# Performance work log

Measured on AMD Instinct MI355X. Metric: run time of the kernel, lower is better.

Reference implementation:

```python
import jax, jax.numpy as jnp
import numpy as np

B = 8192; N = 50; NUM_NODES = 200000; NUM_EDGES = 1000000
FEAT = 64; EFEAT = 4; TD = 16; D = 64


def setup_inputs() -> dict:
    key = jax.random.key(0)
    ks = jax.random.split(key, 32)
    p = lambda i, shape: jax.random.normal(ks[i], shape, jnp.float32) * 0.05
    inp = {}
    nf = jax.random.normal(ks[0], (NUM_NODES, FEAT), jnp.float32)
    skills = jax.random.randint(ks[1], (NUM_NODES,), 0, 100).astype(jnp.float32)
    inp['node_raw_features'] = nf.at[:, 0].set(skills)  # col 0 = skill id
    inp['edge_raw_features'] = jax.random.normal(ks[2], (NUM_EDGES, EFEAT), jnp.float32)
    inp['src_node_ids'] = jax.random.randint(ks[3], (B,), 0, NUM_NODES)
    inp['dst_node_ids'] = jax.random.randint(ks[4], (B,), 0, NUM_NODES)
    inp['node_interact_times'] = jax.random.uniform(ks[5], (B,), jnp.float32, 0.0, 1e4)
    inp['src_neighbor_node_ids'] = jax.random.randint(ks[6], (B, N), 0, NUM_NODES)
    inp['src_neighbor_edge_ids'] = jax.random.randint(ks[7], (B, N), 0, NUM_EDGES)
    inp['src_neighbor_times'] = jax.random.uniform(ks[8], (B, N), jnp.float32, 0.0, 1e4)
    inp['dst_neighbor_node_ids'] = jax.random.randint(ks[9], (B, N), 0, NUM_NODES)
    inp['dst_neighbor_edge_ids'] = jax.random.randint(ks[10], (B, N), 0, NUM_EDGES)
    inp['dst_neighbor_times'] = jax.random.uniform(ks[11], (B, N), jnp.float32, 0.0, 1e4)
    # projection layers
    inp['W_feat'] = p(12, (FEAT, D)); inp['b_feat'] = p(13, (D,))
    inp['W_edge'] = p(14, (1, D));    inp['b_edge'] = p(15, (D,))
    inp['W_time'] = p(16, (TD, D));   inp['b_time'] = p(17, (D,))
    inp['W_struct'] = p(18, (1, D));  inp['b_struct'] = p(19, (D,))
    inp['W_out'] = p(20, (D, D));     inp['b_out'] = p(21, (D,))
    # time encoder (cos(w*dt + b), trainable Linear(1, TD) as in TGN TimeEncoder)
    inp['time_w'] = p(22, (TD,)); inp['time_b'] = p(23, (TD,))
    # src / dst GRUs (PyTorch layout: W_ih [3H,E], W_hh [3H,H])
    inp['src_W_ih'] = p(24, (3 * D, D)); inp['src_W_hh'] = p(25, (3 * D, D))
    inp['src_b_ih'] = p(26, (3 * D,));   inp['src_b_hh'] = p(27, (3 * D,))
    inp['dst_W_ih'] = p(28, (3 * D, D)); inp['dst_W_hh'] = p(29, (3 * D, D))
    inp['dst_b_ih'] = p(30, (3 * D,));   inp['dst_b_hh'] = p(31, (3 * D,))
    return inp


def _lin(x, W, b):
    return x @ W + b


def _gru_last_hidden(x, W_ih, W_hh, b_ih, b_hh):
    # x: [B, T, E] -> final hidden state [B, H] (PyTorch GRU equations)
    Bb, _, _ = x.shape
    H = W_hh.shape[1]

    def step(h, xt):
        gi = xt @ W_ih.T + b_ih            # [B, 3H]
        gh = h @ W_hh.T + b_hh             # [B, 3H]
        ir, iz, inn = jnp.split(gi, 3, axis=-1)
        hr, hz, hn = jnp.split(gh, 3, axis=-1)
        r = jax.nn.sigmoid(ir + hr)
        z = jax.nn.sigmoid(iz + hz)
        n = jnp.tanh(inn + r * hn)
        h_new = (1.0 - z) * n + z * h
        return h_new, None

    h0 = jnp.zeros((Bb, H), x.dtype)
    hT, _ = jax.lax.scan(step, h0, jnp.swapaxes(x, 0, 1))
    return hT


def reference(node_raw_features, edge_raw_features, src_node_ids, dst_node_ids,
              node_interact_times, src_neighbor_node_ids, src_neighbor_edge_ids,
              src_neighbor_times, dst_neighbor_node_ids, dst_neighbor_edge_ids,
              dst_neighbor_times, W_feat, b_feat, W_edge, b_edge, W_time, b_time,
              W_struct, b_struct, W_out, b_out, time_w, time_b,
              src_W_ih, src_W_hh, src_b_ih, src_b_hh,
              dst_W_ih, dst_W_hh, dst_b_ih, dst_b_hh):
    t = node_interact_times
    # append the query interaction itself (edge id 0) -> [B, N+1]
    src_nids = jnp.concatenate([src_neighbor_node_ids, src_node_ids[:, None]], 1)
    src_eids = jnp.concatenate([src_neighbor_edge_ids, jnp.zeros_like(src_node_ids)[:, None]], 1)
    src_ts = jnp.concatenate([src_neighbor_times, t[:, None]], 1)
    dst_nids = jnp.concatenate([dst_neighbor_node_ids, dst_node_ids[:, None]], 1)
    dst_eids = jnp.concatenate([dst_neighbor_edge_ids, jnp.zeros_like(dst_node_ids)[:, None]], 1)
    dst_ts = jnp.concatenate([dst_neighbor_times, t[:, None]], 1)

    # co-occurrence features [B, N, 1]
    co_src = (src_neighbor_node_ids == dst_node_ids[:, None]).astype(jnp.float32)[..., None]
    co_dst = (dst_neighbor_node_ids == src_node_ids[:, None]).astype(jnp.float32)[..., None]
    # skill match features [B, N, 1]
    src_skill = node_raw_features[src_nids][:, :-1, 0].astype(jnp.int32)
    dst_skill = node_raw_features[dst_nids][:, -1, 0].astype(jnp.int32)[:, None]
    skill_f = (src_skill == dst_skill).astype(jnp.float32)[..., None]

    src_struct = _lin(co_src, W_struct, b_struct)
    dst_struct = _lin(co_dst, W_struct, b_struct)
    skill_struct = _lin(skill_f, W_struct, b_struct)

    def get_feats(nids, eids, ts):
        node_f = _lin(node_raw_features[nids], W_feat, b_feat)        # [B,N+1,D]
        delta = t[:, None] - ts                                       # dual-decay ablation: delta times
        tenc = jnp.cos(delta[..., None] * time_w + time_b)            # [B,N+1,TD]
        time_f = _lin(tenc, W_time, b_time)                           # [B,N+1,D]
        edge_f = _lin(edge_raw_features[eids][..., :1], W_edge, b_edge)
        return node_f, edge_f, time_f

    sn, se, st = get_feats(src_nids, src_eids, src_ts)
    dn, de, dt = get_feats(dst_nids, dst_eids, dst_ts)
    src_feats = sn + se + st
    dst_feats = dn + de + dt

    src_emb = _gru_last_hidden(src_feats[:, :-1] + skill_struct + src_struct,
                               src_W_ih, src_W_hh, src_b_ih, src_b_hh) + (se + st)[:, -1]
    dst_emb = _gru_last_hidden((de + dt)[:, :-1] + dst_struct,
                               dst_W_ih, dst_W_hh, dst_b_ih, dst_b_hh) + dst_feats[:, -1]

    return _lin(src_emb, W_out, b_out), _lin(dst_emb, W_out, b_out)
```

## Files before the change

kernel.cpp:

```cpp
#include <hip/hip_runtime.h>
#include <stdint.h>

#define BB 8192
#define NN 50

typedef _Float16 half8 __attribute__((ext_vector_type(8)));
typedef float floatx4 __attribute__((ext_vector_type(4)));

union FragU { uint4 u; half8 h; };
static __device__ __forceinline__ half8 u2h(uint4 u) { FragU f; f.u = u; return f.h; }

static __device__ __forceinline__ uint32_t pk2u(float a, float b) {
    auto p = __builtin_amdgcn_cvt_pkrtz(a, b);
    uint32_t u; __builtin_memcpy(&u, &p, 4); return u;
}

#define MFMA(A, B, C) __builtin_amdgcn_mfma_f32_16x16x32_f16((A), (B), (C), 0, 0, 0)

static __device__ __forceinline__ float frcp(float x) {
#if __has_builtin(__builtin_amdgcn_rcpf)
    return __builtin_amdgcn_rcpf(x);
#else
    return 1.0f / x;
#endif
}
static __device__ __forceinline__ float fexp2(float x) {
#if __has_builtin(__builtin_amdgcn_exp2f)
    return __builtin_amdgcn_exp2f(x);
#else
    return __expf(0.69314718056f * x);
#endif
}
static __device__ __forceinline__ float fsig(float x)   { return frcp(1.0f + fexp2(-1.44269504089f * x)); }
static __device__ __forceinline__ float ftanhf(float x) { return 1.0f - 2.0f * frcp(fexp2(2.88539008178f * x) + 1.0f); }

static __device__ __forceinline__ void bar_lds() {
    asm volatile("s_waitcnt lgkmcnt(0)" ::: "memory");
    __builtin_amdgcn_s_barrier();
}

__global__ __launch_bounds__(128, 2)
void dygkt4(const float* __restrict__ nodef, const float* __restrict__ edgef,
            const int* __restrict__ src_ids, const int* __restrict__ dst_ids,
            const float* __restrict__ times,
            const int* __restrict__ s_nids, const int* __restrict__ s_eids,
            const float* __restrict__ s_ts,
            const int* __restrict__ d_nids, const int* __restrict__ d_eids,
            const float* __restrict__ d_ts,
            const float* __restrict__ W_feat, const float* __restrict__ b_feat,
            const float* __restrict__ W_edge, const float* __restrict__ b_edge,
            const float* __restrict__ W_time, const float* __restrict__ b_time,
            const float* __restrict__ W_str,  const float* __restrict__ b_str,
            const float* __restrict__ W_out,  const float* __restrict__ b_out,
            const float* __restrict__ time_w, const float* __restrict__ time_b,
            const float* __restrict__ sWih, const float* __restrict__ sWhh,
            const float* __restrict__ sbih, const float* __restrict__ sbhh,
            const float* __restrict__ dWih, const float* __restrict__ dWhh,
            const float* __restrict__ dbih, const float* __restrict__ dbhh,
            float* __restrict__ out)
{
    __shared__ uint4 wfA[8][64];
    __shared__ uint4 woA[8][64];
    __shared__ __align__(16) _Float16 xls[2][16 * 72];
    __shared__ __align__(16) _Float16 hls[2][16 * 72];

    const int tid = threadIdx.x, w = tid >> 6, lane = tid & 63;
    const int g = lane >> 4, i16 = lane & 15;
    const bool is_src = blockIdx.x < 512;
    const int ib0 = (int)(blockIdx.x & 511) * 16;
    const int b = ib0 + i16;

    for (int q = tid; q < 512; q += 128) {
        int l = q & 63, tt = q >> 6;
        int kh = tt >> 2, mt = tt & 3, gg = l >> 4, ii = l & 15;
        float v[8], u[8];
        #pragma unroll
        for (int j = 0; j < 8; ++j) {
            int k = 32 * kh + 8 * gg + j, m = 16 * mt + ii;
            v[j] = W_feat[k * 64 + m];
            u[j] = W_out[k * 64 + m];
        }
        wfA[tt][l] = make_uint4(pk2u(v[0],v[1]), pk2u(v[2],v[3]), pk2u(v[4],v[5]), pk2u(v[6],v[7]));
        woA[tt][l] = make_uint4(pk2u(u[0],u[1]), pk2u(u[2],u[3]), pk2u(u[4],u[5]), pk2u(u[6],u[7]));
    }
    for (int q = tid; q < 16 * 72 / 2; q += 128) ((uint32_t*)hls[0])[q] = 0u;
    __syncthreads();

    const float* WI = is_src ? sWih : dWih;
    const float* WH = is_src ? sWhh : dWhh;
    uint4 wih[6][2], whh[6][2];
    #pragma unroll
    for (int gt = 0; gt < 3; ++gt)
        #pragma unroll
        for (int tq = 0; tq < 2; ++tq)
            #pragma unroll
            for (int kh = 0; kh < 2; ++kh) {
                int row = 64 * gt + 16 * (2 * w + tq) + i16;
                const float* p = WI + (size_t)row * 64 + 32 * kh + 8 * g;
                float4 a = *(const float4*)p, c = *(const float4*)(p + 4);
                wih[gt * 2 + tq][kh] = make_uint4(pk2u(a.x,a.y), pk2u(a.z,a.w), pk2u(c.x,c.y), pk2u(c.z,c.w));
                const float* qq = WH + (size_t)row * 64 + 32 * kh + 8 * g;
                float4 e = *(const float4*)qq, f = *(const float4*)(qq + 4);
                whh[gt * 2 + tq][kh] = make_uint4(pk2u(e.x,e.y), pk2u(e.z,e.w), pk2u(f.x,f.y), pk2u(f.z,f.w));
            }

    uint4 wtA[2];
    #pragma unroll
    for (int tq = 0; tq < 2; ++tq) {
        int mt = 2 * w + tq;
        float v[8];
        #pragma unroll
        for (int j = 0; j < 8; ++j) {
            int k = 8 * g + j, dim = 16 * mt + i16;
            float x = 0.0f;
            if (k < 16)       x = W_time[k * 64 + dim];
            else if (k == 16) x = W_edge[dim];
            else if (k == 17) x = W_str[dim];
            else if (k == 18) x = b_edge[dim] + b_time[dim];
            else if (k == 19) x = is_src ? (b_feat[dim] + 2.0f * b_str[dim]) : b_str[dim];
            else if (k == 20) x = b_feat[dim];
            v[j] = x;
        }
        wtA[tq] = make_uint4(pk2u(v[0],v[1]), pk2u(v[2],v[3]), pk2u(v[4],v[5]), pk2u(v[6],v[7]));
    }

    const float* BI = is_src ? sbih : dbih;
    const float* BH = is_src ? sbhh : dbhh;
    floatx4 brz[4], bin[2], bhn[2];
    #pragma unroll
    for (int gz = 0; gz < 2; ++gz)
        #pragma unroll
        for (int tq = 0; tq < 2; ++tq) {
            int r0 = 64 * gz + 16 * (2 * w + tq) + 4 * g;
            floatx4 v;
            #pragma unroll
            for (int r = 0; r < 4; ++r) v[r] = BI[r0 + r] + BH[r0 + r];
            brz[gz * 2 + tq] = v;
        }
    #pragma unroll
    for (int tq = 0; tq < 2; ++tq) {
        int r0 = 128 + 16 * (2 * w + tq) + 4 * g;
        floatx4 vi, vh;
        #pragma unroll
        for (int r = 0; r < 4; ++r) { vi[r] = BI[r0 + r]; vh[r] = BH[r0 + r]; }
        bin[tq] = vi; bhn[tq] = vh;
    }

    const int* pn = (is_src ? s_nids : d_nids) + (size_t)b * NN;
    const int* pe = (is_src ? s_eids : d_eids) + (size_t)b * NN;
    const float* pt = (is_src ? s_ts : d_ts) + (size_t)b * NN;
    const float tqL = times[b];
    const int didL = dst_ids[b];
    const int oid = is_src ? didL : src_ids[b];
    const float dskill = is_src ? nodef[(size_t)didL * 64] : 0.0f;
    float twc[8], tbc[8];
    #pragma unroll
    for (int j = 0; j < 8; ++j) {
        int k = 8 * (g & 1) + j;
        twc[j] = time_w[k]; tbc[j] = time_b[k];
    }

    int nidC = pn[0], eidC = pe[0];
    float tsC = pt[0];
    float e0C = edgef[4 * (size_t)eidC];
    float4 nfa = {0,0,0,0}, nfb = {0,0,0,0}, nfc = {0,0,0,0}, nfd = {0,0,0,0};
    if (is_src) {
        const float* rp = nodef + (size_t)nidC * 64 + 8 * g;
        nfa = *(const float4*)rp;        nfb = *(const float4*)(rp + 4);
        nfc = *(const float4*)(rp + 32); nfd = *(const float4*)(rp + 36);
    }

    floatx4 hM[2] = {{0,0,0,0},{0,0,0,0}};
    const floatx4 z4 = {0,0,0,0};
    int cur = 0;

    for (int t = 0; t < NN; ++t) {
        int nidN = 0, eidN = 0; float tsN = 0.0f;
        if (t + 1 < NN) { nidN = pn[t + 1]; eidN = pe[t + 1]; tsN = pt[t + 1]; }

        float nsk = __shfl(nfa.x, i16);
        float sf = ((nidC == oid) ? 1.0f : 0.0f) +
                   ((is_src && nsk == dskill) ? 1.0f : 0.0f);
        float delta = tqL - tsC;
        uint4 tb4;
        if (g < 2) {
            float cv[8];
            #pragma unroll
            for (int j = 0; j < 8; ++j) cv[j] = __cosf(delta * twc[j] + tbc[j]);
            tb4 = make_uint4(pk2u(cv[0],cv[1]), pk2u(cv[2],cv[3]), pk2u(cv[4],cv[5]), pk2u(cv[6],cv[7]));
        } else if (g == 2) {
            tb4 = make_uint4(pk2u(e0C, sf), pk2u(1.0f, 1.0f), 0u, 0u);
        } else {
            tb4 = make_uint4(0u, 0u, 0u, 0u);
        }
        half8 tB = u2h(tb4);

        floatx4 xacc[2];
        if (is_src) {
            uint4 nf0 = make_uint4(pk2u(nfa.x,nfa.y), pk2u(nfa.z,nfa.w), pk2u(nfb.x,nfb.y), pk2u(nfb.z,nfb.w));
            uint4 nf1 = make_uint4(pk2u(nfc.x,nfc.y), pk2u(nfc.z,nfc.w), pk2u(nfd.x,nfd.y), pk2u(nfd.z,nfd.w));
            half8 nB0 = u2h(nf0), nB1 = u2h(nf1);
            #pragma unroll
            for (int tq = 0; tq < 2; ++tq) {
                int mt = 2 * w + tq;
                floatx4 a = MFMA(u2h(wfA[mt][lane]), nB0, z4);
                a = MFMA(u2h(wfA[4 + mt][lane]), nB1, a);
                xacc[tq] = MFMA(u2h(wtA[tq]), tB, a);
            }
        } else {
            #pragma unroll
            for (int tq = 0; tq < 2; ++tq) xacc[tq] = MFMA(u2h(wtA[tq]), tB, z4);
        }

        #pragma unroll
        for (int tq = 0; tq < 2; ++tq)
            *(uint2*)&xls[cur][i16 * 72 + 32 * w + 16 * tq + 4 * g] =
                make_uint2(pk2u(xacc[tq][0], xacc[tq][1]), pk2u(xacc[tq][2], xacc[tq][3]));

        float e0N = 0.0f; float4 na = {0,0,0,0}, nb = {0,0,0,0}, nc = {0,0,0,0}, nd = {0,0,0,0};
        if (t + 1 < NN) {
            e0N = edgef[4 * (size_t)eidN];
            if (is_src) {
                const float* rp = nodef + (size_t)nidN * 64 + 8 * g;
                na = *(const float4*)rp;        nb = *(const float4*)(rp + 4);
                nc = *(const float4*)(rp + 32); nd = *(const float4*)(rp + 36);
            }
        }

        bar_lds();

        half8 xB0 = u2h(*(const uint4*)&xls[cur][i16 * 72 + 8 * g]);
        half8 xB1 = u2h(*(const uint4*)&xls[cur][i16 * 72 + 32 + 8 * g]);
        half8 hB0 = u2h(*(const uint4*)&hls[cur][i16 * 72 + 8 * g]);
        half8 hB1 = u2h(*(const uint4*)&hls[cur][i16 * 72 + 32 + 8 * g]);

        floatx4 rg[2], zg[2], ia[2], ha[2];
        #pragma unroll
        for (int tq = 0; tq < 2; ++tq) {
            floatx4 a = MFMA(u2h(wih[tq][0]), xB0, brz[tq]);
            a = MFMA(u2h(wih[tq][1]), xB1, a);
            a = MFMA(u2h(whh[tq][0]), hB0, a);
            rg[tq] = MFMA(u2h(whh[tq][1]), hB1, a);
        }
        #pragma unroll
        for (int tq = 0; tq < 2; ++tq) {
            floatx4 a = MFMA(u2h(wih[2 + tq][0]), xB0, brz[2 + tq]);
            a = MFMA(u2h(wih[2 + tq][1]), xB1, a);
            a = MFMA(u2h(whh[2 + tq][0]), hB0, a);
            zg[tq] = MFMA(u2h(whh[2 + tq][1]), hB1, a);
        }
        #pragma unroll
        for (int tq = 0; tq < 2; ++tq) {
            floatx4 a = MFMA(u2h(wih[4 + tq][0]), xB0, bin[tq]);
            ia[tq] = MFMA(u2h(wih[4 + tq][1]), xB1, a);
            floatx4 c = MFMA(u2h(whh[4 + tq][0]), hB0, bhn[tq]);
            ha[tq] = MFMA(u2h(whh[4 + tq][1]), hB1, c);
        }

        #pragma unroll
        for (int tq = 0; tq < 2; ++tq)
            #pragma unroll
            for (int r = 0; r < 4; ++r) {
                float rr = fsig(rg[tq][r]);
                float zz = fsig(zg[tq][r]);
                float nn = ftanhf(ia[tq][r] + rr * ha[tq][r]);
                hM[tq][r] = nn + zz * (hM[tq][r] - nn);
            }

        #pragma unroll
        for (int tq = 0; tq < 2; ++tq)
            *(uint2*)&hls[cur ^ 1][i16 * 72 + 32 * w + 16 * tq + 4 * g] =
                make_uint2(pk2u(hM[tq][0], hM[tq][1]), pk2u(hM[tq][2], hM[tq][3]));

        cur ^= 1;
        nidC = nidN; eidC = eidN; tsC = tsN; e0C = e0N;
        nfa = na; nfb = nb; nfc = nc; nfd = nd;
    }

    float e00 = edgef[0];
    uint4 tt4;
    if (g < 2) {
        float cv[8];
        #pragma unroll
        for (int j = 0; j < 8; ++j) cv[j] = __cosf(tbc[j]);
        tt4 = make_uint4(pk2u(cv[0],cv[1]), pk2u(cv[2],cv[3]), pk2u(cv[4],cv[5]), pk2u(cv[6],cv[7]));
    } else if (g == 2) {
        tt4 = make_uint4(pk2u(e00, 0.0f), pk2u(1.0f, 0.0f), pk2u(is_src ? 0.0f : 1.0f, 0.0f), 0u);
    } else {
        tt4 = make_uint4(0u, 0u, 0u, 0u);
    }
    half8 tT = u2h(tt4);

    floatx4 tacc[2];
    #pragma unroll
    for (int tq = 0; tq < 2; ++tq) tacc[tq] = MFMA(u2h(wtA[tq]), tT, z4);
    if (!is_src) {
        const float* rp = nodef + (size_t)didL * 64 + 8 * g;
        float4 da = *(const float4*)rp,        db = *(const float4*)(rp + 4);
        float4 dc = *(const float4*)(rp + 32), dd = *(const float4*)(rp + 36);
        uint4 d0 = make_uint4(pk2u(da.x,da.y), pk2u(da.z,da.w), pk2u(db.x,db.y), pk2u(db.z,db.w));
        uint4 d1 = make_uint4(pk2u(dc.x,dc.y), pk2u(dc.z,dc.w), pk2u(dd.x,dd.y), pk2u(dd.z,dd.w));
        #pragma unroll
        for (int tq = 0; tq < 2; ++tq) {
            int mt = 2 * w + tq;
            tacc[tq] = MFMA(u2h(wfA[mt][lane]), u2h(d0), tacc[tq]);
            tacc[tq] = MFMA(u2h(wfA[4 + mt][lane]), u2h(d1), tacc[tq]);
        }
    }

    #pragma unroll
    for (int tq = 0; tq < 2; ++tq) {
        floatx4 e = hM[tq] + tacc[tq];
        *(uint2*)&xls[0][i16 * 72 + 32 * w + 16 * tq + 4 * g] =
            make_uint2(pk2u(e[0], e[1]), pk2u(e[2], e[3]));
    }
    bar_lds();
    half8 eB0 = u2h(*(const uint4*)&xls[0][i16 * 72 + 8 * g]);
    half8 eB1 = u2h(*(const uint4*)&xls[0][i16 * 72 + 32 + 8 * g]);

    const size_t obase = (is_src ? 0 : (size_t)BB * 64) + (size_t)b * 64;
    #pragma unroll
    for (int tq = 0; tq < 2; ++tq) {
        int mt = 2 * w + tq;
        floatx4 bo;
        #pragma unroll
        for (int r = 0; r < 4; ++r) bo[r] = b_out[16 * mt + 4 * g + r];
        floatx4 o = MFMA(u2h(woA[mt][lane]), eB0, bo);
        o = MFMA(u2h(woA[4 + mt][lane]), eB1, o);
        *(floatx4*)(out + obase + 16 * mt + 4 * g) = o;
    }
}

extern "C" void kernel_launch(void* const* d_in, const int* in_sizes, int n_in,
                              void* d_out, int out_size, void* d_ws, size_t ws_size,
                              hipStream_t stream) {
    (void)in_sizes; (void)n_in; (void)d_ws; (void)ws_size; (void)out_size;
    const float* nodef  = (const float*)d_in[0];
    const float* edgef  = (const float*)d_in[1];
    const int*   srcid  = (const int*)  d_in[2];
    const int*   dstid  = (const int*)  d_in[3];
    const float* times  = (const float*)d_in[4];
    const int*   s_nids = (const int*)  d_in[5];
    const int*   s_eids = (const int*)  d_in[6];
    const float* s_ts   = (const float*)d_in[7];
    const int*   d_nids = (const int*)  d_in[8];
    const int*   d_eids = (const int*)  d_in[9];
    const float* d_ts   = (const float*)d_in[10];
    const float* W_feat = (const float*)d_in[11];
    const float* b_feat = (const float*)d_in[12];
    const float* W_edge = (const float*)d_in[13];
    const float* b_edge = (const float*)d_in[14];
    const float* W_time = (const float*)d_in[15];
    const float* b_time = (const float*)d_in[16];
    const float* W_str  = (const float*)d_in[17];
    const float* b_str  = (const float*)d_in[18];
    const float* W_out  = (const float*)d_in[19];
    const float* b_out  = (const float*)d_in[20];
    const float* time_w = (const float*)d_in[21];
    const float* time_b = (const float*)d_in[22];
    const float* sWih   = (const float*)d_in[23];
    const float* sWhh   = (const float*)d_in[24];
    const float* sbih   = (const float*)d_in[25];
    const float* sbhh   = (const float*)d_in[26];
    const float* dWih   = (const float*)d_in[27];
    const float* dWhh   = (const float*)d_in[28];
    const float* dbih   = (const float*)d_in[29];
    const float* dbhh   = (const float*)d_in[30];

    dim3 grid(1024), block(128);
    dygkt4<<<grid, block, 0, stream>>>(
        nodef, edgef, srcid, dstid, times,
        s_nids, s_eids, s_ts, d_nids, d_eids, d_ts,
        W_feat, b_feat, W_edge, b_edge, W_time, b_time,
        W_str, b_str, W_out, b_out, time_w, time_b,
        sWih, sWhh, sbih, sbhh, dWih, dWhh, dbih, dbhh,
        (float*)d_out);
}
```

Measured before the change: 245.5 us.

## Split GRU output tiles across four waves per block and hold projection weights in registers

The block grows from 2 to 4 waves, so each wave now owns a single 16-wide output tile instead of two. That halves the MFMA chain and the gate math each wave runs per serial GRU timestep, and gives more waves per CU to hide the gather latency. The W_feat and W_out fragments move out of LDS and into registers, and W_out is loaded only at the end. Src and dst blocks are now interleaved by block index. In exchange, every wave repeats the node and edge gathers and the time encoding, and the per-step barriers now synchronize four waves instead of two.

Result: slower. 556.2 us (+126.6%).

```diff
diff --git a/kernel.cpp b/kernel.cpp
--- a/kernel.cpp
+++ b/kernel.cpp
@@ -39,8 +39,8 @@
     __builtin_amdgcn_s_barrier();
 }
 
-__global__ __launch_bounds__(128, 2)
-void dygkt4(const float* __restrict__ nodef, const float* __restrict__ edgef,
+__global__ __launch_bounds__(256, 4)
+void dygkt5(const float* __restrict__ nodef, const float* __restrict__ edgef,
             const int* __restrict__ src_ids, const int* __restrict__ dst_ids,
             const float* __restrict__ times,
             const int* __restrict__ s_nids, const int* __restrict__ s_eids,
@@ -59,59 +59,51 @@
             const float* __restrict__ dbih, const float* __restrict__ dbhh,
             float* __restrict__ out)
 {
-    __shared__ uint4 wfA[8][64];
-    __shared__ uint4 woA[8][64];
     __shared__ __align__(16) _Float16 xls[2][16 * 72];
     __shared__ __align__(16) _Float16 hls[2][16 * 72];
 
     const int tid = threadIdx.x, w = tid >> 6, lane = tid & 63;
     const int g = lane >> 4, i16 = lane & 15;
-    const bool is_src = blockIdx.x < 512;
-    const int ib0 = (int)(blockIdx.x & 511) * 16;
-    const int b = ib0 + i16;
-
-    for (int q = tid; q < 512; q += 128) {
-        int l = q & 63, tt = q >> 6;
-        int kh = tt >> 2, mt = tt & 3, gg = l >> 4, ii = l & 15;
+    const bool is_src = (blockIdx.x & 1) == 0;
+    const int b = (int)(blockIdx.x >> 1) * 16 + i16;
+
+    for (int q = tid; q < 16 * 72 / 2; q += 256) ((uint32_t*)hls[0])[q] = 0u;
+
+    uint4 wf0, wf1;
+    {
         float v[8], u[8];
         #pragma unroll
         for (int j = 0; j < 8; ++j) {
-            int k = 32 * kh + 8 * gg + j, m = 16 * mt + ii;
-            v[j] = W_feat[k * 64 + m];
-            u[j] = W_out[k * 64 + m];
-        }
-        wfA[tt][l] = make_uint4(pk2u(v[0],v[1]), pk2u(v[2],v[3]), pk2u(v[4],v[5]), pk2u(v[6],v[7]));
-        woA[tt][l] = make_uint4(pk2u(u[0],u[1]), pk2u(u[2],u[3]), pk2u(u[4],u[5]), pk2u(u[6],u[7]));
-    }
-    for (int q = tid; q < 16 * 72 / 2; q += 128) ((uint32_t*)hls[0])[q] = 0u;
-    __syncthreads();
+            int m = 16 * w + i16;
+            v[j] = W_feat[(8 * g + j) * 64 + m];
+            u[j] = W_feat[(32 + 8 * g + j) * 64 + m];
+        }
+        wf0 = make_uint4(pk2u(v[0],v[1]), pk2u(v[2],v[3]), pk2u(v[4],v[5]), pk2u(v[6],v[7]));
+        wf1 = make_uint4(pk2u(u[0],u[1]), pk2u(u[2],u[3]), pk2u(u[4],u[5]), pk2u(u[6],u[7]));
+    }
 
     const float* WI = is_src ? sWih : dWih;
     const float* WH = is_src ? sWhh : dWhh;
-    uint4 wih[6][2], whh[6][2];
+    uint4 wih[3][2], whh[3][2];
     #pragma unroll
     for (int gt = 0; gt < 3; ++gt)
         #pragma unroll
-        for (int tq = 0; tq < 2; ++tq)
-            #pragma unroll
-            for (int kh = 0; kh < 2; ++kh) {
-                int row = 64 * gt + 16 * (2 * w + tq) + i16;
-                const float* p = WI + (size_t)row * 64 + 32 * kh + 8 * g;
-                float4 a = *(const float4*)p, c = *(const float4*)(p + 4);
-                wih[gt * 2 + tq][kh] = make_uint4(pk2u(a.x,a.y), pk2u(a.z,a.w), pk2u(c.x,c.y), pk2u(c.z,c.w));
-                const float* qq = WH + (size_t)row * 64 + 32 * kh + 8 * g;
-                float4 e = *(const float4*)qq, f = *(const float4*)(qq + 4);
-                whh[gt * 2 + tq][kh] = make_uint4(pk2u(e.x,e.y), pk2u(e.z,e.w), pk2u(f.x,f.y), pk2u(f.z,f.w));
-            }
-
-    uint4 wtA[2];
-    #pragma unroll
-    for (int tq = 0; tq < 2; ++tq) {
-        int mt = 2 * w + tq;
+        for (int kh = 0; kh < 2; ++kh) {
+            int row = 64 * gt + 16 * w + i16;
+            const float* p = WI + (size_t)row * 64 + 32 * kh + 8 * g;
+            float4 a = *(const float4*)p, c = *(const float4*)(p + 4);
+            wih[gt][kh] = make_uint4(pk2u(a.x,a.y), pk2u(a.z,a.w), pk2u(c.x,c.y), pk2u(c.z,c.w));
+            const float* qq = WH + (size_t)row * 64 + 32 * kh + 8 * g;
+            float4 e = *(const float4*)qq, f = *(const float4*)(qq + 4);
+            whh[gt][kh] = make_uint4(pk2u(e.x,e.y), pk2u(e.z,e.w), pk2u(f.x,f.y), pk2u(f.z,f.w));
+        }
+
+    uint4 wtA;
+    {
         float v[8];
         #pragma unroll
         for (int j = 0; j < 8; ++j) {
-            int k = 8 * g + j, dim = 16 * mt + i16;
+            int k = 8 * g + j, dim = 16 * w + i16;
             float x = 0.0f;
             if (k < 16)       x = W_time[k * 64 + dim];
             else if (k == 16) x = W_edge[dim];
@@ -121,29 +113,24 @@
             else if (k == 20) x = b_feat[dim];
             v[j] = x;
         }
-        wtA[tq] = make_uint4(pk2u(v[0],v[1]), pk2u(v[2],v[3]), pk2u(v[4],v[5]), pk2u(v[6],v[7]));
+        wtA = make_uint4(pk2u(v[0],v[1]), pk2u(v[2],v[3]), pk2u(v[4],v[5]), pk2u(v[6],v[7]));
     }
 
     const float* BI = is_src ? sbih : dbih;
     const float* BH = is_src ? sbhh : dbhh;
-    floatx4 brz[4], bin[2], bhn[2];
+    floatx4 brz[2], bin, bhn;
     #pragma unroll
-    for (int gz = 0; gz < 2; ++gz)
-        #pragma unroll
-        for (int tq = 0; tq < 2; ++tq) {
-            int r0 = 64 * gz + 16 * (2 * w + tq) + 4 * g;
-            floatx4 v;
-            #pragma unroll
-            for (int r = 0; r < 4; ++r) v[r] = BI[r0 + r] + BH[r0 + r];
-            brz[gz * 2 + tq] = v;
-        }
-    #pragma unroll
-    for (int tq = 0; tq < 2; ++tq) {
-        int r0 = 128 + 16 * (2 * w + tq) + 4 * g;
-        floatx4 vi, vh;
-        #pragma unroll
-        for (int r = 0; r < 4; ++r) { vi[r] = BI[r0 + r]; vh[r] = BH[r0 + r]; }
-        bin[tq] = vi; bhn[tq] = vh;
+    for (int gz = 0; gz < 2; ++gz) {
+        int r0 = 64 * gz + 16 * w + 4 * g;
+        floatx4 v;
+        #pragma unroll
+        for (int r = 0; r < 4; ++r) v[r] = BI[r0 + r] + BH[r0 + r];
+        brz[gz] = v;
+    }
+    {
+        int r0 = 128 + 16 * w + 4 * g;
+        #pragma unroll
+        for (int r = 0; r < 4; ++r) { bin[r] = BI[r0 + r]; bhn[r] = BH[r0 + r]; }
     }
 
     const int* pn = (is_src ? s_nids : d_nids) + (size_t)b * NN;
@@ -160,6 +147,8 @@
         twc[j] = time_w[k]; tbc[j] = time_b[k];
     }
 
+    __syncthreads();
+
     int nidC = pn[0], eidC = pe[0];
     float tsC = pt[0];
     float e0C = edgef[4 * (size_t)eidC];
@@ -170,7 +159,7 @@
         nfc = *(const float4*)(rp + 32); nfd = *(const float4*)(rp + 36);
     }
 
-    floatx4 hM[2] = {{0,0,0,0},{0,0,0,0}};
+    floatx4 hM = {0,0,0,0};
     const floatx4 z4 = {0,0,0,0};
     int cur = 0;
 
@@ -195,27 +184,19 @@
         }
         half8 tB = u2h(tb4);
 
-        floatx4 xacc[2];
+        floatx4 xacc;
         if (is_src) {
             uint4 nf0 = make_uint4(pk2u(nfa.x,nfa.y), pk2u(nfa.z,nfa.w), pk2u(nfb.x,nfb.y), pk2u(nfb.z,nfb.w));
             uint4 nf1 = make_uint4(pk2u(nfc.x,nfc.y), pk2u(nfc.z,nfc.w), pk2u(nfd.x,nfd.y), pk2u(nfd.z,nfd.w));
-            half8 nB0 = u2h(nf0), nB1 = u2h(nf1);
-            #pragma unroll
-            for (int tq = 0; tq < 2; ++tq) {
-                int mt = 2 * w + tq;
-                floatx4 a = MFMA(u2h(wfA[mt][lane]), nB0, z4);
-                a = MFMA(u2h(wfA[4 + mt][lane]), nB1, a);
-                xacc[tq] = MFMA(u2h(wtA[tq]), tB, a);
-            }
+            floatx4 a = MFMA(u2h(wf0), u2h(nf0), z4);
+            a = MFMA(u2h(wf1), u2h(nf1), a);
+            xacc = MFMA(u2h(wtA), tB, a);
         } else {
-            #pragma unroll
-            for (int tq = 0; tq < 2; ++tq) xacc[tq] = MFMA(u2h(wtA[tq]), tB, z4);
-        }
-
-        #pragma unroll
-        for (int tq = 0; tq < 2; ++tq)
-            *(uint2*)&xls[cur][i16 * 72 + 32 * w + 16 * tq + 4 * g] =
-                make_uint2(pk2u(xacc[tq][0], xacc[tq][1]), pk2u(xacc[tq][2], xacc[tq][3]));
+            xacc = MFMA(u2h(wtA), tB, z4);
+        }
+
+        *(uint2*)&xls[cur][i16 * 72 + 16 * w + 4 * g] =
+            make_uint2(pk2u(xacc[0], xacc[1]), pk2u(xacc[2], xacc[3]));
 
         float e0N = 0.0f; float4 na = {0,0,0,0}, nb = {0,0,0,0}, nc = {0,0,0,0}, nd = {0,0,0,0};
         if (t + 1 < NN) {
@@ -234,43 +215,36 @@
         half8 hB0 = u2h(*(const uint4*)&hls[cur][i16 * 72 + 8 * g]);
         half8 hB1 = u2h(*(const uint4*)&hls[cur][i16 * 72 + 32 + 8 * g]);
 
-        floatx4 rg[2], zg[2], ia[2], ha[2];
-        #pragma unroll
-        for (int tq = 0; tq < 2; ++tq) {
-            floatx4 a = MFMA(u2h(wih[tq][0]), xB0, brz[tq]);
-            a = MFMA(u2h(wih[tq][1]), xB1, a);
-            a = MFMA(u2h(whh[tq][0]), hB0, a);
-            rg[tq] = MFMA(u2h(whh[tq][1]), hB1, a);
-        }
-        #pragma unroll
-        for (int tq = 0; tq < 2; ++tq) {
-            floatx4 a = MFMA(u2h(wih[2 + tq][0]), xB0, brz[2 + tq]);
-            a = MFMA(u2h(wih[2 + tq][1]), xB1, a);
-            a = MFMA(u2h(whh[2 + tq][0]), hB0, a);
-            zg[tq] = MFMA(u2h(whh[2 + tq][1]), hB1, a);
-        }
-        #pragma unroll
-        for (int tq = 0; tq < 2; ++tq) {
-            floatx4 a = MFMA(u2h(wih[4 + tq][0]), xB0, bin[tq]);
-            ia[tq] = MFMA(u2h(wih[4 + tq][1]), xB1, a);
-            floatx4 c = MFMA(u2h(whh[4 + tq][0]), hB0, bhn[tq]);
-            ha[tq] = MFMA(u2h(whh[4 + tq][1]), hB1, c);
-        }
-
-        #pragma unroll
-        for (int tq = 0; tq < 2; ++tq)
-            #pragma unroll
-            for (int r = 0; r < 4; ++r) {
-                float rr = fsig(rg[tq][r]);
-                float zz = fsig(zg[tq][r]);
-                float nn = ftanhf(ia[tq][r] + rr * ha[tq][r]);
-                hM[tq][r] = nn + zz * (hM[tq][r] - nn);
-            }
-
-        #pragma unroll
-        for (int tq = 0; tq < 2; ++tq)
-            *(uint2*)&hls[cur ^ 1][i16 * 72 + 32 * w + 16 * tq + 4 * g] =
-                make_uint2(pk2u(hM[tq][0], hM[tq][1]), pk2u(hM[tq][2], hM[tq][3]));
+        floatx4 rg, zg, ia, ha;
+        {
+            floatx4 a = MFMA(u2h(wih[0][0]), xB0, brz[0]);
+            a = MFMA(u2h(wih[0][1]), xB1, a);
+            a = MFMA(u2h(whh[0][0]), hB0, a);
+            rg = MFMA(u2h(whh[0][1]), hB1, a);
+        }
+        {
+            floatx4 a = MFMA(u2h(wih[1][0]), xB0, brz[1]);
+            a = MFMA(u2h(wih[1][1]), xB1, a);
+            a = MFMA(u2h(whh[1][0]), hB0, a);
+            zg = MFMA(u2h(whh[1][1]), hB1, a);
+        }
+        {
+            floatx4 a = MFMA(u2h(wih[2][0]), xB0, bin);
+            ia = MFMA(u2h(wih[2][1]), xB1, a);
+            floatx4 c = MFMA(u2h(whh[2][0]), hB0, bhn);
+            ha = MFMA(u2h(whh[2][1]), hB1, c);
+        }
+
+        #pragma unroll
+        for (int r = 0; r < 4; ++r) {
+            float rr = fsig(rg[r]);
+            float zz = fsig(zg[r]);
+            float nn = ftanhf(ia[r] + rr * ha[r]);
+            hM[r] = nn + zz * (hM[r] - nn);
+        }
+
+        *(uint2*)&hls[cur ^ 1][i16 * 72 + 16 * w + 4 * g] =
+            make_uint2(pk2u(hM[0], hM[1]), pk2u(hM[2], hM[3]));
 
         cur ^= 1;
         nidC = nidN; eidC = eidN; tsC = tsN; e0C = e0N;
@@ -291,27 +265,33 @@
     }
     half8 tT = u2h(tt4);
 
-    floatx4 tacc[2];
-    #pragma unroll
-    for (int tq = 0; tq < 2; ++tq) tacc[tq] = MFMA(u2h(wtA[tq]), tT, z4);
+    floatx4 tacc = MFMA(u2h(wtA), tT, z4);
     if (!is_src) {
         const float* rp = nodef + (size_t)didL * 64 + 8 * g;
         float4 da = *(const float4*)rp,        db = *(const float4*)(rp + 4);
         float4 dc = *(const float4*)(rp + 32), dd = *(const float4*)(rp + 36);
         uint4 d0 = make_uint4(pk2u(da.x,da.y), pk2u(da.z,da.w), pk2u(db.x,db.y), pk2u(db.z,db.w));
         uint4 d1 = make_uint4(pk2u(dc.x,dc.y), pk2u(dc.z,dc.w), pk2u(dd.x,dd.y), pk2u(dd.z,dd.w));
-        #pragma unroll
-        for (int tq = 0; tq < 2; ++tq) {
-            int mt = 2 * w + tq;
-            tacc[tq] = MFMA(u2h(wfA[mt][lane]), u2h(d0), tacc[tq]);
-            tacc[tq] = MFMA(u2h(wfA[4 + mt][lane]), u2h(d1), tacc[tq]);
-        }
-    }
-
-    #pragma unroll
-    for (int tq = 0; tq < 2; ++tq) {
-        floatx4 e = hM[tq] + tacc[tq];
-        *(uint2*)&xls[0][i16 * 72 + 32 * w + 16 * tq + 4 * g] =
+        tacc = MFMA(u2h(wf0), u2h(d0), tacc);
+        tacc = MFMA(u2h(wf1), u2h(d1), tacc);
+    }
+
+    uint4 wo0, wo1;
+    {
+        float v[8], u[8];
+        #pragma unroll
+        for (int j = 0; j < 8; ++j) {
+            int m = 16 * w + i16;
+            v[j] = W_out[(8 * g + j) * 64 + m];
+            u[j] = W_out[(32 + 8 * g + j) * 64 + m];
+        }
+        wo0 = make_uint4(pk2u(v[0],v[1]), pk2u(v[2],v[3]), pk2u(v[4],v[5]), pk2u(v[6],v[7]));
+        wo1 = make_uint4(pk2u(u[0],u[1]), pk2u(u[2],u[3]), pk2u(u[4],u[5]), pk2u(u[6],u[7]));
+    }
+
+    {
+        floatx4 e = hM + tacc;
+        *(uint2*)&xls[0][i16 * 72 + 16 * w + 4 * g] =
             make_uint2(pk2u(e[0], e[1]), pk2u(e[2], e[3]));
     }
     bar_lds();
@@ -319,15 +299,13 @@
     half8 eB1 = u2h(*(const uint4*)&xls[0][i16 * 72 + 32 + 8 * g]);
 
     const size_t obase = (is_src ? 0 : (size_t)BB * 64) + (size_t)b * 64;
-    #pragma unroll
-    for (int tq = 0; tq < 2; ++tq) {
-        int mt = 2 * w + tq;
+    {
         floatx4 bo;
         #pragma unroll
-        for (int r = 0; r < 4; ++r) bo[r] = b_out[16 * mt + 4 * g + r];
-        floatx4 o = MFMA(u2h(woA[mt][lane]), eB0, bo);
-        o = MFMA(u2h(woA[4 + mt][lane]), eB1, o);
-        *(floatx4*)(out + obase + 16 * mt + 4 * g) = o;
+        for (int r = 0; r < 4; ++r) bo[r] = b_out[16 * w + 4 * g + r];
+        floatx4 o = MFMA(u2h(wo0), eB0, bo);
+        o = MFMA(u2h(wo1), eB1, o);
+        *(floatx4*)(out + obase + 16 * w + 4 * g) = o;
     }
 }
 
@@ -367,8 +345,8 @@
     const float* dbih   = (const float*)d_in[29];
     const float* dbhh   = (const float*)d_in[30];
 
-    dim3 grid(1024), block(128);
-    dygkt4<<<grid, block, 0, stream>>>(
+    dim3 grid(1024), block(256);
+    dygkt5<<<grid, block, 0, stream>>>(
         nodef, edgef, srcid, dstid, times,
         s_nids, s_eids, s_ts, d_nids, d_eids, d_ts,
         W_feat, b_feat, W_edge, b_edge, W_time, b_time,
```

## Software-pipeline GRU input projection one step ahead and prescale gate weights

Applied to the files above, without the earlier changes.

Restructures the GRU recurrence so the input-side gate projections for step t+1 are computed right after step t's hidden update. Only the hidden-side MFMAs stay on the serial critical path. Gate weights and biases are prescaled by the exp2 sigmoid/tanh constants, which removes multiplies from the activation math. W_ih fragments move to LDS, W_feat/W_out move to registers, and blocks interleave src/dst. The cost is a deeper prefetch pipeline, extra LDS traffic per step and a different register/LDS balance that may affect occupancy.

Result: slower. 259.7 us (+5.8%).

```diff
diff --git a/kernel.cpp b/kernel.cpp
--- a/kernel.cpp
+++ b/kernel.cpp
@@ -31,8 +31,6 @@
     return __expf(0.69314718056f * x);
 #endif
 }
-static __device__ __forceinline__ float fsig(float x)   { return frcp(1.0f + fexp2(-1.44269504089f * x)); }
-static __device__ __forceinline__ float ftanhf(float x) { return 1.0f - 2.0f * frcp(fexp2(2.88539008178f * x) + 1.0f); }
 
 static __device__ __forceinline__ void bar_lds() {
     asm volatile("s_waitcnt lgkmcnt(0)" ::: "memory");
@@ -40,7 +38,7 @@
 }
 
 __global__ __launch_bounds__(128, 2)
-void dygkt4(const float* __restrict__ nodef, const float* __restrict__ edgef,
+void dygkt7(const float* __restrict__ nodef, const float* __restrict__ edgef,
             const int* __restrict__ src_ids, const int* __restrict__ dst_ids,
             const float* __restrict__ times,
             const int* __restrict__ s_nids, const int* __restrict__ s_eids,
@@ -59,38 +57,38 @@
             const float* __restrict__ dbih, const float* __restrict__ dbhh,
             float* __restrict__ out)
 {
-    __shared__ uint4 wfA[8][64];
-    __shared__ uint4 woA[8][64];
     __shared__ __align__(16) _Float16 xls[2][16 * 72];
     __shared__ __align__(16) _Float16 hls[2][16 * 72];
+    __shared__ uint4 wihL[2][12][64];
 
     const int tid = threadIdx.x, w = tid >> 6, lane = tid & 63;
     const int g = lane >> 4, i16 = lane & 15;
-    const bool is_src = blockIdx.x < 512;
-    const int ib0 = (int)(blockIdx.x & 511) * 16;
-    const int b = ib0 + i16;
-
-    for (int q = tid; q < 512; q += 128) {
-        int l = q & 63, tt = q >> 6;
-        int kh = tt >> 2, mt = tt & 3, gg = l >> 4, ii = l & 15;
-        float v[8], u[8];
-        #pragma unroll
-        for (int j = 0; j < 8; ++j) {
-            int k = 32 * kh + 8 * gg + j, m = 16 * mt + ii;
-            v[j] = W_feat[k * 64 + m];
-            u[j] = W_out[k * 64 + m];
-        }
-        wfA[tt][l] = make_uint4(pk2u(v[0],v[1]), pk2u(v[2],v[3]), pk2u(v[4],v[5]), pk2u(v[6],v[7]));
-        woA[tt][l] = make_uint4(pk2u(u[0],u[1]), pk2u(u[2],u[3]), pk2u(u[4],u[5]), pk2u(u[6],u[7]));
-    }
+    const bool is_src = (blockIdx.x & 1) == 0;
+    const int b = (int)(blockIdx.x >> 1) * 16 + i16;
+
+    const float SRZ = -1.44269504089f;
+    const float SN  =  2.88539008178f;
+
     for (int q = tid; q < 16 * 72 / 2; q += 128) ((uint32_t*)hls[0])[q] = 0u;
-    __syncthreads();
+
+    uint4 wf[2][2];
+    #pragma unroll
+    for (int tq = 0; tq < 2; ++tq)
+        #pragma unroll
+        for (int kh = 0; kh < 2; ++kh) {
+            float v[8];
+            #pragma unroll
+            for (int j = 0; j < 8; ++j)
+                v[j] = W_feat[(32 * kh + 8 * g + j) * 64 + 16 * (2 * w + tq) + i16];
+            wf[tq][kh] = make_uint4(pk2u(v[0],v[1]), pk2u(v[2],v[3]), pk2u(v[4],v[5]), pk2u(v[6],v[7]));
+        }
 
     const float* WI = is_src ? sWih : dWih;
     const float* WH = is_src ? sWhh : dWhh;
-    uint4 wih[6][2], whh[6][2];
-    #pragma unroll
-    for (int gt = 0; gt < 3; ++gt)
+    uint4 whh[6][2];
+    #pragma unroll
+    for (int gt = 0; gt < 3; ++gt) {
+        const float s = (gt == 2) ? SN : SRZ;
         #pragma unroll
         for (int tq = 0; tq < 2; ++tq)
             #pragma unroll
@@ -98,11 +96,14 @@
                 int row = 64 * gt + 16 * (2 * w + tq) + i16;
                 const float* p = WI + (size_t)row * 64 + 32 * kh + 8 * g;
                 float4 a = *(const float4*)p, c = *(const float4*)(p + 4);
-                wih[gt * 2 + tq][kh] = make_uint4(pk2u(a.x,a.y), pk2u(a.z,a.w), pk2u(c.x,c.y), pk2u(c.z,c.w));
+                wihL[w][gt * 4 + tq * 2 + kh][lane] =
+                    make_uint4(pk2u(s*a.x,s*a.y), pk2u(s*a.z,s*a.w), pk2u(s*c.x,s*c.y), pk2u(s*c.z,s*c.w));
                 const float* qq = WH + (size_t)row * 64 + 32 * kh + 8 * g;
                 float4 e = *(const float4*)qq, f = *(const float4*)(qq + 4);
-                whh[gt * 2 + tq][kh] = make_uint4(pk2u(e.x,e.y), pk2u(e.z,e.w), pk2u(f.x,f.y), pk2u(f.z,f.w));
-            }
+                whh[gt * 2 + tq][kh] =
+                    make_uint4(pk2u(s*e.x,s*e.y), pk2u(s*e.z,s*e.w), pk2u(s*f.x,s*f.y), pk2u(s*f.z,s*f.w));
+            }
+    }
 
     uint4 wtA[2];
     #pragma unroll
@@ -134,7 +135,7 @@
             int r0 = 64 * gz + 16 * (2 * w + tq) + 4 * g;
             floatx4 v;
             #pragma unroll
-            for (int r = 0; r < 4; ++r) v[r] = BI[r0 + r] + BH[r0 + r];
+            for (int r = 0; r < 4; ++r) v[r] = SRZ * (BI[r0 + r] + BH[r0 + r]);
             brz[gz * 2 + tq] = v;
         }
     #pragma unroll
@@ -142,7 +143,7 @@
         int r0 = 128 + 16 * (2 * w + tq) + 4 * g;
         floatx4 vi, vh;
         #pragma unroll
-        for (int r = 0; r < 4; ++r) { vi[r] = BI[r0 + r]; vh[r] = BH[r0 + r]; }
+        for (int r = 0; r < 4; ++r) { vi[r] = SN * BI[r0 + r]; vh[r] = SN * BH[r0 + r]; }
         bin[tq] = vi; bhn[tq] = vh;
     }
 
@@ -160,6 +161,8 @@
         twc[j] = time_w[k]; tbc[j] = time_b[k];
     }
 
+    __syncthreads();
+
     int nidC = pn[0], eidC = pe[0];
     float tsC = pt[0];
     float e0C = edgef[4 * (size_t)eidC];
@@ -169,15 +172,21 @@
         nfa = *(const float4*)rp;        nfb = *(const float4*)(rp + 4);
         nfc = *(const float4*)(rp + 32); nfd = *(const float4*)(rp + 36);
     }
-
+    int nidN = pn[1], eidN = pe[1];
+    float tsN = pt[1];
+    float e0N = edgef[4 * (size_t)eidN];
+    float4 na = {0,0,0,0}, nb = {0,0,0,0}, nc = {0,0,0,0}, nd = {0,0,0,0};
+    if (is_src) {
+        const float* rp = nodef + (size_t)nidN * 64 + 8 * g;
+        na = *(const float4*)rp;        nb = *(const float4*)(rp + 4);
+        nc = *(const float4*)(rp + 32); nd = *(const float4*)(rp + 36);
+    }
+
+    const floatx4 z4 = {0,0,0,0};
+    floatx4 gr[2], gz_[2], gn[2];
     floatx4 hM[2] = {{0,0,0,0},{0,0,0,0}};
-    const floatx4 z4 = {0,0,0,0};
-    int cur = 0;
-
-    for (int t = 0; t < NN; ++t) {
-        int nidN = 0, eidN = 0; float tsN = 0.0f;
-        if (t + 1 < NN) { nidN = pn[t + 1]; eidN = pe[t + 1]; tsN = pt[t + 1]; }
-
+
+    {
         float nsk = __shfl(nfa.x, i16);
         float sf = ((nidC == oid) ? 1.0f : 0.0f) +
                    ((is_src && nsk == dskill) ? 1.0f : 0.0f);
@@ -194,31 +203,78 @@
             tb4 = make_uint4(0u, 0u, 0u, 0u);
         }
         half8 tB = u2h(tb4);
-
-        floatx4 xacc[2];
-        if (is_src) {
-            uint4 nf0 = make_uint4(pk2u(nfa.x,nfa.y), pk2u(nfa.z,nfa.w), pk2u(nfb.x,nfb.y), pk2u(nfb.z,nfb.w));
-            uint4 nf1 = make_uint4(pk2u(nfc.x,nfc.y), pk2u(nfc.z,nfc.w), pk2u(nfd.x,nfd.y), pk2u(nfd.z,nfd.w));
-            half8 nB0 = u2h(nf0), nB1 = u2h(nf1);
+        #pragma unroll
+        for (int tq = 0; tq < 2; ++tq) {
+            floatx4 xacc;
+            if (is_src) {
+                uint4 nf0 = make_uint4(pk2u(nfa.x,nfa.y), pk2u(nfa.z,nfa.w), pk2u(nfb.x,nfb.y), pk2u(nfb.z,nfb.w));
+                uint4 nf1 = make_uint4(pk2u(nfc.x,nfc.y), pk2u(nfc.z,nfc.w), pk2u(nfd.x,nfd.y), pk2u(nfd.z,nfd.w));
+                floatx4 a = MFMA(u2h(wf[tq][0]), u2h(nf0), z4);
+                a = MFMA(u2h(wf[tq][1]), u2h(nf1), a);
+                xacc = MFMA(u2h(wtA[tq]), tB, a);
+            } else {
+                xacc = MFMA(u2h(wtA[tq]), tB, z4);
+            }
+            *(uint2*)&xls[0][i16 * 72 + 32 * w + 16 * tq + 4 * g] =
+                make_uint2(pk2u(xacc[0], xacc[1]), pk2u(xacc[2], xacc[3]));
+        }
+        bar_lds();
+        half8 xB0 = u2h(*(const uint4*)&xls[0][i16 * 72 + 8 * g]);
+        half8 xB1 = u2h(*(const uint4*)&xls[0][i16 * 72 + 32 + 8 * g]);
+        #pragma unroll
+        for (int tq = 0; tq < 2; ++tq) {
+            floatx4 a = MFMA(u2h(wihL[w][0 + tq * 2 + 0][lane]), xB0, brz[tq]);
+            gr[tq]    = MFMA(u2h(wihL[w][0 + tq * 2 + 1][lane]), xB1, a);
+            floatx4 c = MFMA(u2h(wihL[w][4 + tq * 2 + 0][lane]), xB0, brz[2 + tq]);
+            gz_[tq]   = MFMA(u2h(wihL[w][4 + tq * 2 + 1][lane]), xB1, c);
+            floatx4 e = MFMA(u2h(wihL[w][8 + tq * 2 + 0][lane]), xB0, bin[tq]);
+            gn[tq]    = MFMA(u2h(wihL[w][8 + tq * 2 + 1][lane]), xB1, e);
+        }
+    }
+
+    int cur = 0;
+    for (int t = 0; t < NN; ++t) {
+        const bool hasx = (t + 1 < NN);
+
+        nidC = nidN; eidC = eidN; tsC = tsN; e0C = e0N;
+        nfa = na; nfb = nb; nfc = nc; nfd = nd;
+
+        if (hasx) {
+            float nsk = __shfl(nfa.x, i16);
+            float sf = ((nidC == oid) ? 1.0f : 0.0f) +
+                       ((is_src && nsk == dskill) ? 1.0f : 0.0f);
+            float delta = tqL - tsC;
+            uint4 tb4;
+            if (g < 2) {
+                float cv[8];
+                #pragma unroll
+                for (int j = 0; j < 8; ++j) cv[j] = __cosf(delta * twc[j] + tbc[j]);
+                tb4 = make_uint4(pk2u(cv[0],cv[1]), pk2u(cv[2],cv[3]), pk2u(cv[4],cv[5]), pk2u(cv[6],cv[7]));
+            } else if (g == 2) {
+                tb4 = make_uint4(pk2u(e0C, sf), pk2u(1.0f, 1.0f), 0u, 0u);
+            } else {
+                tb4 = make_uint4(0u, 0u, 0u, 0u);
+            }
+            half8 tB = u2h(tb4);
             #pragma unroll
             for (int tq = 0; tq < 2; ++tq) {
-                int mt = 2 * w + tq;
-                floatx4 a = MFMA(u2h(wfA[mt][lane]), nB0, z4);
-                a = MFMA(u2h(wfA[4 + mt][lane]), nB1, a);
-                xacc[tq] = MFMA(u2h(wtA[tq]), tB, a);
-            }
-        } else {
-            #pragma unroll
-            for (int tq = 0; tq < 2; ++tq) xacc[tq] = MFMA(u2h(wtA[tq]), tB, z4);
-        }
-
-        #pragma unroll
-        for (int tq = 0; tq < 2; ++tq)
-            *(uint2*)&xls[cur][i16 * 72 + 32 * w + 16 * tq + 4 * g] =
-                make_uint2(pk2u(xacc[tq][0], xacc[tq][1]), pk2u(xacc[tq][2], xacc[tq][3]));
-
-        float e0N = 0.0f; float4 na = {0,0,0,0}, nb = {0,0,0,0}, nc = {0,0,0,0}, nd = {0,0,0,0};
-        if (t + 1 < NN) {
+                floatx4 xacc;
+                if (is_src) {
+                    uint4 nf0 = make_uint4(pk2u(nfa.x,nfa.y), pk2u(nfa.z,nfa.w), pk2u(nfb.x,nfb.y), pk2u(nfb.z,nfb.w));
+                    uint4 nf1 = make_uint4(pk2u(nfc.x,nfc.y), pk2u(nfc.z,nfc.w), pk2u(nfd.x,nfd.y), pk2u(nfd.z,nfd.w));
+                    floatx4 a = MFMA(u2h(wf[tq][0]), u2h(nf0), z4);
+                    a = MFMA(u2h(wf[tq][1]), u2h(nf1), a);
+                    xacc = MFMA(u2h(wtA[tq]), tB, a);
+                } else {
+                    xacc = MFMA(u2h(wtA[tq]), tB, z4);
+                }
+                *(uint2*)&xls[cur ^ 1][i16 * 72 + 32 * w + 16 * tq + 4 * g] =
+                    make_uint2(pk2u(xacc[0], xacc[1]), pk2u(xacc[2], xacc[3]));
+            }
+        }
+
+        if (t + 2 < NN) {
+            nidN = pn[t + 2]; eidN = pe[t + 2]; tsN = pt[t + 2];
             e0N = edgef[4 * (size_t)eidN];
             if (is_src) {
                 const float* rp = nodef + (size_t)nidN * 64 + 8 * g;
@@ -229,41 +285,28 @@
 
         bar_lds();
 
-        half8 xB0 = u2h(*(const uint4*)&xls[cur][i16 * 72 + 8 * g]);
-        half8 xB1 = u2h(*(const uint4*)&xls[cur][i16 * 72 + 32 + 8 * g]);
         half8 hB0 = u2h(*(const uint4*)&hls[cur][i16 * 72 + 8 * g]);
         half8 hB1 = u2h(*(const uint4*)&hls[cur][i16 * 72 + 32 + 8 * g]);
 
-        floatx4 rg[2], zg[2], ia[2], ha[2];
+        floatx4 rg[2], zg[2], ha[2];
         #pragma unroll
         for (int tq = 0; tq < 2; ++tq) {
-            floatx4 a = MFMA(u2h(wih[tq][0]), xB0, brz[tq]);
-            a = MFMA(u2h(wih[tq][1]), xB1, a);
-            a = MFMA(u2h(whh[tq][0]), hB0, a);
-            rg[tq] = MFMA(u2h(whh[tq][1]), hB1, a);
-        }
-        #pragma unroll
-        for (int tq = 0; tq < 2; ++tq) {
-            floatx4 a = MFMA(u2h(wih[2 + tq][0]), xB0, brz[2 + tq]);
-            a = MFMA(u2h(wih[2 + tq][1]), xB1, a);
-            a = MFMA(u2h(whh[2 + tq][0]), hB0, a);
-            zg[tq] = MFMA(u2h(whh[2 + tq][1]), hB1, a);
-        }
-        #pragma unroll
-        for (int tq = 0; tq < 2; ++tq) {
-            floatx4 a = MFMA(u2h(wih[4 + tq][0]), xB0, bin[tq]);
-            ia[tq] = MFMA(u2h(wih[4 + tq][1]), xB1, a);
-            floatx4 c = MFMA(u2h(whh[4 + tq][0]), hB0, bhn[tq]);
-            ha[tq] = MFMA(u2h(whh[4 + tq][1]), hB1, c);
+            floatx4 a = MFMA(u2h(whh[tq][0]), hB0, gr[tq]);
+            rg[tq]    = MFMA(u2h(whh[tq][1]), hB1, a);
+            floatx4 c = MFMA(u2h(whh[2 + tq][0]), hB0, gz_[tq]);
+            zg[tq]    = MFMA(u2h(whh[2 + tq][1]), hB1, c);
+            floatx4 e = MFMA(u2h(whh[4 + tq][0]), hB0, bhn[tq]);
+            ha[tq]    = MFMA(u2h(whh[4 + tq][1]), hB1, e);
         }
 
         #pragma unroll
         for (int tq = 0; tq < 2; ++tq)
             #pragma unroll
             for (int r = 0; r < 4; ++r) {
-                float rr = fsig(rg[tq][r]);
-                float zz = fsig(zg[tq][r]);
-                float nn = ftanhf(ia[tq][r] + rr * ha[tq][r]);
+                float rr = frcp(1.0f + fexp2(rg[tq][r]));
+                float zz = frcp(1.0f + fexp2(zg[tq][r]));
+                float vv = gn[tq][r] + rr * ha[tq][r];
+                float nn = 1.0f - 2.0f * frcp(fexp2(vv) + 1.0f);
                 hM[tq][r] = nn + zz * (hM[tq][r] - nn);
             }
 
@@ -272,9 +315,21 @@
             *(uint2*)&hls[cur ^ 1][i16 * 72 + 32 * w + 16 * tq + 4 * g] =
                 make_uint2(pk2u(hM[tq][0], hM[tq][1]), pk2u(hM[tq][2], hM[tq][3]));
 
+        if (hasx) {
+            half8 xB0 = u2h(*(const uint4*)&xls[cur ^ 1][i16 * 72 + 8 * g]);
+            half8 xB1 = u2h(*(const uint4*)&xls[cur ^ 1][i16 * 72 + 32 + 8 * g]);
+            #pragma unroll
+            for (int tq = 0; tq < 2; ++tq) {
+                floatx4 a = MFMA(u2h(wihL[w][0 + tq * 2 + 0][lane]), xB0, brz[tq]);
+                gr[tq]    = MFMA(u2h(wihL[w][0 + tq * 2 + 1][lane]), xB1, a);
+                floatx4 c = MFMA(u2h(wihL[w][4 + tq * 2 + 0][lane]), xB0, brz[2 + tq]);
+                gz_[tq]   = MFMA(u2h(wihL[w][4 + tq * 2 + 1][lane]), xB1, c);
+                floatx4 e = MFMA(u2h(wihL[w][8 + tq * 2 + 0][lane]), xB0, bin[tq]);
+                gn[tq]    = MFMA(u2h(wihL[w][8 + tq * 2 + 1][lane]), xB1, e);
+            }
+        }
+
         cur ^= 1;
-        nidC = nidN; eidC = eidN; tsC = tsN; e0C = e0N;
-        nfa = na; nfb = nb; nfc = nc; nfd = nd;
     }
 
     float e00 = edgef[0];
@@ -302,11 +357,22 @@
         uint4 d1 = make_uint4(pk2u(dc.x,dc.y), pk2u(dc.z,dc.w), pk2u(dd.x,dd.y), pk2u(dd.z,dd.w));
         #pragma unroll
         for (int tq = 0; tq < 2; ++tq) {
-            int mt = 2 * w + tq;
-            tacc[tq] = MFMA(u2h(wfA[mt][lane]), u2h(d0), tacc[tq]);
-            tacc[tq] = MFMA(u2h(wfA[4 + mt][lane]), u2h(d1), tacc[tq]);
-        }
-    }
+            tacc[tq] = MFMA(u2h(wf[tq][0]), u2h(d0), tacc[tq]);
+            tacc[tq] = MFMA(u2h(wf[tq][1]), u2h(d1), tacc[tq]);
+        }
+    }
+
+    uint4 wo[2][2];
+    #pragma unroll
+    for (int tq = 0; tq < 2; ++tq)
+        #pragma unroll
+        for (int kh = 0; kh < 2; ++kh) {
+            float v[8];
+            #pragma unroll
+            for (int j = 0; j < 8; ++j)
+                v[j] = W_out[(32 * kh + 8 * g + j) * 64 + 16 * (2 * w + tq) + i16];
+            wo[tq][kh] = make_uint4(pk2u(v[0],v[1]), pk2u(v[2],v[3]), pk2u(v[4],v[5]), pk2u(v[6],v[7]));
+        }
 
     #pragma unroll
     for (int tq = 0; tq < 2; ++tq) {
@@ -321,13 +387,12 @@
     const size_t obase = (is_src ? 0 : (size_t)BB * 64) + (size_t)b * 64;
     #pragma unroll
     for (int tq = 0; tq < 2; ++tq) {
-        int mt = 2 * w + tq;
         floatx4 bo;
         #pragma unroll
-        for (int r = 0; r < 4; ++r) bo[r] = b_out[16 * mt + 4 * g + r];
-        floatx4 o = MFMA(u2h(woA[mt][lane]), eB0, bo);
-        o = MFMA(u2h(woA[4 + mt][lane]), eB1, o);
-        *(floatx4*)(out + obase + 16 * mt + 4 * g) = o;
+        for (int r = 0; r < 4; ++r) bo[r] = b_out[16 * (2 * w + tq) + 4 * g + r];
+        floatx4 o = MFMA(u2h(wo[tq][0]), eB0, bo);
+        o = MFMA(u2h(wo[tq][1]), eB1, o);
+        *(floatx4*)(out + obase + 16 * (2 * w + tq) + 4 * g) = o;
     }
 }
 
@@ -368,7 +433,7 @@
     const float* dbhh   = (const float*)d_in[30];
 
     dim3 grid(1024), block(128);
-    dygkt4<<<grid, block, 0, stream>>>(
+    dygkt7<<<grid, block, 0, stream>>>(
         nodef, edgef, srcid, dstid, times,
         s_nids, s_eids, s_ts, d_nids, d_eids, d_ts,
         W_feat, b_feat, W_edge, b_edge, W_time, b_time,
```
